# Optimization experiments

Hardware: AMD Instinct MI355X
Metric: run time of the kernel (lower is better)

The kernel has to match this reference:

```python
import jax, jax.numpy as jnp
import numpy as np
from jax import lax

C = 64
K = 3
RED = 8


def _lrelu(x):
    return jax.nn.leaky_relu(x, 0.1)


def setup_inputs() -> dict:
    key = jax.random.key(0)
    ks = jax.random.split(key, 8)
    b, h, w = 32, 128, 128
    x0 = jax.random.normal(ks[0], (b, C, h, w), dtype=jnp.float32)
    v = jax.random.normal(ks[1], (b, C), dtype=jnp.float32)
    s = 0.05
    # CA layer: two 1x1 convs (no bias) acting on the [b,64] embedding
    ca_w1 = jax.random.normal(ks[2], (C // RED, C), dtype=jnp.float32) * s
    ca_w2 = jax.random.normal(ks[3], (C, C // RED), dtype=jnp.float32) * s
    # kernel-generating MLP: Linear(64,64) -> LeakyReLU -> Linear(64, 64*K*K), no bias
    k_w1 = jax.random.normal(ks[4], (C, C), dtype=jnp.float32) * s
    k_w2 = jax.random.normal(ks[5], (C * K * K, C), dtype=jnp.float32) * s
    # final 1x1 conv (default_conv, bias=True)
    conv_w = jax.random.normal(ks[6], (C, C), dtype=jnp.float32) * s
    conv_b = jax.random.normal(ks[7], (C,), dtype=jnp.float32) * s
    return {"x0": x0, "v": v, "ca_w1": ca_w1, "ca_w2": ca_w2,
            "k_w1": k_w1, "k_w2": k_w2, "conv_w": conv_w, "conv_b": conv_b}


def reference(x0, v, ca_w1, ca_w2, k_w1, k_w2, conv_w, conv_b):
    b, c, h, w = x0.shape
    # Channel attention: sigmoid(W2 @ lrelu(W1 @ v)) gates x0 per (b,c)
    att = jax.nn.sigmoid(_lrelu(v @ ca_w1.T) @ ca_w2.T)  # [b, c]
    out = x0 * att[:, :, None, None]
    # Per-sample, per-channel K x K kernels generated from the embedding
    kern = (_lrelu(v @ k_w1.T) @ k_w2.T).reshape(b * c, 1, K, K)
    p = (K - 1) // 2
    y = lax.conv_general_dilated(
        out.reshape(1, b * c, h, w), kern,
        window_strides=(1, 1), padding=[(p, p), (p, p)],
        feature_group_count=b * c,
        dimension_numbers=("NCHW", "OIHW", "NCHW"))
    y = _lrelu(y).reshape(b, c, h, w)
    # final 1x1 conv with bias
    return jnp.einsum("bchw,oc->bohw", y, conv_w) + conv_b[None, :, None, None]
```

## Files before the change

kernel.cpp:

```cpp
#include <hip/hip_runtime.h>

#define HW 128
#define XBb 16
#define XBf 4
#define KTb 24592
#define LDS_BYTES 26896

typedef __attribute__((ext_vector_type(8))) short  bfrag;
typedef __attribute__((ext_vector_type(16))) float f16x;
typedef __attribute__((ext_vector_type(4)))  float f4;

__device__ __forceinline__ float lrelu(float x) { return x > 0.f ? x : 0.1f * x; }

__device__ __forceinline__ short f2bf(float f) {
    unsigned u = __builtin_bit_cast(unsigned, f);
    u = u + 0x7FFFu + ((u >> 16) & 1u);
    return (short)(u >> 16);
}

__device__ float g_ktab[32 * 768];
__device__ short g_whi[4096];

__global__ __launch_bounds__(64) void dgfem_prep(
    const float* __restrict__ v, const float* __restrict__ ca_w1,
    const float* __restrict__ ca_w2, const float* __restrict__ k_w1,
    const float* __restrict__ k_w2, const float* __restrict__ conv_w)
{
    const int b = blockIdx.x;
    const int t = threadIdx.x;

    if (b == 32) {
        for (int i = t; i < 4096; i += 64) g_whi[i] = f2bf(conv_w[i]);
        return;
    }

    __shared__ float vb[64], t1[8], att[64], t2[64];
    vb[t] = v[b * 64 + t];
    __syncthreads();

    if (t < 8) {
        float s = 0.f;
        for (int j = 0; j < 64; ++j) s += vb[j] * ca_w1[t * 64 + j];
        t1[t] = lrelu(s);
    }
    {
        float s = 0.f;
        for (int j = 0; j < 64; ++j) s += vb[j] * k_w1[t * 64 + j];
        t2[t] = lrelu(s);
    }
    __syncthreads();
    {
        float s = 0.f;
        for (int i = 0; i < 8; ++i) s += t1[i] * ca_w2[t * 8 + i];
        att[t] = 1.f / (1.f + expf(-s));
    }
    __syncthreads();
    for (int r = t; r < 576; r += 64) {
        int c = r / 9, tp = r - c * 9;
        float s = 0.f;
        for (int j = 0; j < 64; ++j) s += t2[j] * k_w2[r * 64 + j];
        int m = c >> 4, g = (c >> 3) & 1, a = (c >> 2) & 1, j2 = c & 3;
        int row = ((m * 2 + a) * 2 + g) * 4 + j2;
        int dst = (tp < 4) ? (row * 4 + tp)
                : (tp < 8) ? (256 + row * 4 + (tp - 4))
                           : (512 + row);
        g_ktab[b * 768 + dst] = s * att[c];
    }
}

__global__ __launch_bounds__(256) void dgfem_main(
    const float* __restrict__ x0, const float* __restrict__ conv_b,
    float* __restrict__ out)
{
    const int t  = threadIdx.x;
    const int w  = t >> 6;
    const int l  = t & 63;
    const int g  = l >> 5;
    const int ln = l & 31;
    const int px = w * 32 + ln;

    const int bid  = blockIdx.x;
    const int orig = (bid & 7) * 512 + (bid >> 3);
    const int b    = orig >> 7;
    const int gy   = orig & 127;

    __shared__ __align__(16) char lds[LDS_BYTES];
    float* ldsf = (float*)lds;

    {
        const float* ksrc = g_ktab + b * 768;
        const float rm0 = (gy > 0)   ? 1.f : 0.f;
        const float rm2 = (gy < 127) ? 1.f : 0.f;
        for (int i = t; i < 576; i += 256) {
            float rm;
            if (i < 256)      rm = ((i & 3) < 3) ? rm0 : 1.f;
            else if (i < 512) rm = ((i & 3) < 2) ? 1.f : rm2;
            else              rm = rm2;
            *(float*)(lds + KTb + i * 4) = ksrc[i] * rm;
        }
    }

    const int doff = w * 1024 + l * 16;
    int inv0, inv1, inv2;
    {
        #pragma unroll
        for (int q = 0; q < 3; ++q) {
            int F      = q * 4096 + doff;
            int slot   = F / 1536;
            int within = F - slot * 1536;
            int rowq   = gy - 1 + (within >> 9);
            int crow   = min(max(rowq, 0), 127);
            int gs = slot >> 2, j2s = slot & 3;
            int iv = (gs * 8 + j2s) * 65536 + crow * 512 + (within & 511);
            if (q == 0) inv0 = iv; else if (q == 1) inv1 = iv; else inv2 = iv;
        }
    }

    const char* xb = (const char*)x0 + ((size_t)b << 22);

    #define STAGE(rr_, sel_)                                                   \
    {                                                                          \
        const char* srcb = xb + ((size_t)(((rr_) >> 1) * 16 + ((rr_) & 1) * 4) << 16); \
        char* dstb = lds + XBb + (sel_) * 12288 + doff;                        \
        __builtin_amdgcn_global_load_lds(                                      \
            (const __attribute__((address_space(1))) unsigned*)(srcb + inv0),  \
            (__attribute__((address_space(3))) unsigned*)(dstb), 16, 0, 0);    \
        __builtin_amdgcn_global_load_lds(                                      \
            (const __attribute__((address_space(1))) unsigned*)(srcb + inv1),  \
            (__attribute__((address_space(3))) unsigned*)(dstb + 4096), 16, 0, 0); \
        __builtin_amdgcn_global_load_lds(                                      \
            (const __attribute__((address_space(1))) unsigned*)(srcb + inv2),  \
            (__attribute__((address_space(3))) unsigned*)(dstb + 8192), 16, 0, 0); \
    }

    f16x acc0, acc1;
    #pragma unroll
    for (int i = 0; i < 16; ++i) { acc0[i] = 0.f; acc1[i] = 0.f; }

    const float mLf = (px > 0)   ? 1.f : 0.f;
    const float mRf = (px < 127) ? 1.f : 0.f;

    bfrag yh;
    bfrag whi0, whi1;
    const char* const wbase = (const char*)g_whi + ln * 128 + g * 16;

    STAGE(0, 0);
    __syncthreads();

    #define ROUND(rr_, a_, m_, sel_)                                           \
    {                                                                          \
        if (!(a_)) {                                                           \
            whi0 = *(const bfrag*)(wbase + (m_) * 32);                         \
            whi1 = *(const bfrag*)(wbase + (m_) * 32 + 4096);                  \
        }                                                                      \
        if ((rr_) < 7) STAGE((rr_) + 1, (sel_) ^ 1);                           \
        const float* xbase = ldsf + (XBf + (sel_) * 3072 + g * 1536 + px - 1); \
        const int    krowb = ((rr_) * 2 + g) * 4;                              \
        _Pragma("unroll")                                                      \
        for (int j2 = 0; j2 < 4; ++j2) {                                       \
            f4 kA = *(const f4*)(lds + KTb + (krowb + j2) * 16);               \
            f4 kB = *(const f4*)(lds + KTb + 1024 + (krowb + j2) * 16);        \
            float k8v = *(const float*)(lds + KTb + 2048 + (krowb + j2) * 4);  \
            const float* bA = xbase + j2 * 384;                                \
            float xL0 = bA[0]   * mLf, xC0 = bA[1],   xR0 = bA[2]   * mRf;     \
            float xL1 = bA[128] * mLf, xC1 = bA[129], xR1 = bA[130] * mRf;     \
            float xL2 = bA[256] * mLf, xC2 = bA[257], xR2 = bA[258] * mRf;     \
            float aY = fmaf(kA.x, xL0, fmaf(kA.y, xC0, kA.z * xR0))            \
                     + fmaf(kA.w, xL1, fmaf(kB.x, xC1, kB.y * xR1))            \
                     + fmaf(kB.z, xL2, fmaf(kB.w, xC2, k8v  * xR2));           \
            yh[(a_) * 4 + j2] = f2bf(lrelu(aY));                               \
        }                                                                      \
        if (a_) {                                                              \
            acc0 = __builtin_amdgcn_mfma_f32_32x32x16_bf16(whi0, yh, acc0, 0, 0, 0); \
            acc1 = __builtin_amdgcn_mfma_f32_32x32x16_bf16(whi1, yh, acc1, 0, 0, 0); \
        }                                                                      \
        if ((rr_) < 7) __syncthreads();                                        \
    }

    ROUND(0, 0, 0, 0);
    ROUND(1, 1, 0, 1);
    ROUND(2, 0, 1, 0);
    ROUND(3, 1, 1, 1);
    ROUND(4, 0, 2, 0);
    ROUND(5, 1, 2, 1);
    ROUND(6, 0, 3, 0);
    ROUND(7, 1, 3, 1);

    #undef ROUND
    #undef STAGE

    float* ob = out + ((size_t)b << 20) + (size_t)gy * HW + px;
    #pragma unroll
    for (int q = 0; q < 4; ++q) {
        const int obase = 8 * q + 4 * g;
        float4 bv0 = *(const float4*)&conv_b[obase];
        float4 bv1 = *(const float4*)&conv_b[32 + obase];
        const float* b0f = (const float*)&bv0;
        const float* b1f = (const float*)&bv1;
        #pragma unroll
        for (int r2 = 0; r2 < 4; ++r2) {
            ob[(size_t)(obase + r2) * 16384]      = acc0[q * 4 + r2] + b0f[r2];
            ob[(size_t)(32 + obase + r2) * 16384] = acc1[q * 4 + r2] + b1f[r2];
        }
    }
}

extern "C" void kernel_launch(void* const* d_in, const int* in_sizes, int n_in,
                              void* d_out, int out_size, void* d_ws, size_t ws_size,
                              hipStream_t stream) {
    const float* x0     = (const float*)d_in[0];
    const float* v      = (const float*)d_in[1];
    const float* ca_w1  = (const float*)d_in[2];
    const float* ca_w2  = (const float*)d_in[3];
    const float* k_w1   = (const float*)d_in[4];
    const float* k_w2   = (const float*)d_in[5];
    const float* conv_w = (const float*)d_in[6];
    const float* conv_b = (const float*)d_in[7];
    float* outp = (float*)d_out;

    dgfem_prep<<<dim3(33), dim3(64), 0, stream>>>(v, ca_w1, ca_w2, k_w1, k_w2, conv_w);
    dgfem_main<<<dim3(4096), dim3(256), 0, stream>>>(x0, conv_b, outp);
}
```

Measured before the change: 77.54 us.

## Shrink main kernel to single-wave blocks with barrier-free vmcnt pipelining

Each block now handles one 32-pixel segment of a row with a single 64-lane wave instead of four waves covering the whole row, and the grid grows to match. The x tile per stage becomes a 40-column halo window, and __syncthreads are replaced by explicit s_waitcnt vmcnt on the async global-to-LDS loads. The 1x1 conv weight fragments are also loaded into registers up front. The aim is to drop block-wide barriers and cut LDS use to raise occupancy. In exchange, halo columns are loaded redundantly by neighbouring blocks, the loads are narrower (4-byte ones for the tail), and there are more blocks to schedule.

```diff
diff --git a/kernel.cpp b/kernel.cpp
--- a/kernel.cpp
+++ b/kernel.cpp
@@ -1,10 +1,8 @@
 #include <hip/hip_runtime.h>
 
 #define HW 128
-#define XBb 16
-#define XBf 4
-#define KTb 24592
-#define LDS_BYTES 26896
+#define XBB 2304
+#define LDS_BYTES 10016
 
 typedef __attribute__((ext_vector_type(8))) short  bfrag;
 typedef __attribute__((ext_vector_type(16))) float f16x;
@@ -68,21 +66,21 @@
     }
 }
 
-__global__ __launch_bounds__(256) void dgfem_main(
+__global__ __launch_bounds__(64) void dgfem_main(
     const float* __restrict__ x0, const float* __restrict__ conv_b,
     float* __restrict__ out)
 {
-    const int t  = threadIdx.x;
-    const int w  = t >> 6;
-    const int l  = t & 63;
+    const int l  = threadIdx.x;
     const int g  = l >> 5;
     const int ln = l & 31;
-    const int px = w * 32 + ln;
 
     const int bid  = blockIdx.x;
-    const int orig = (bid & 7) * 512 + (bid >> 3);
-    const int b    = orig >> 7;
-    const int gy   = orig & 127;
+    const int orig = (bid & 7) * 2048 + (bid >> 3);
+    const int b    = orig >> 9;
+    const int rem  = orig & 511;
+    const int gy   = rem >> 2;
+    const int px0  = (rem & 3) * 32;
+    const int px   = px0 + ln;
 
     __shared__ __align__(16) char lds[LDS_BYTES];
     float* ldsf = (float*)lds;
@@ -91,28 +89,30 @@
         const float* ksrc = g_ktab + b * 768;
         const float rm0 = (gy > 0)   ? 1.f : 0.f;
         const float rm2 = (gy < 127) ? 1.f : 0.f;
-        for (int i = t; i < 576; i += 256) {
+        for (int i = l; i < 576; i += 64) {
             float rm;
             if (i < 256)      rm = ((i & 3) < 3) ? rm0 : 1.f;
             else if (i < 512) rm = ((i & 3) < 2) ? 1.f : rm2;
             else              rm = rm2;
-            *(float*)(lds + KTb + i * 4) = ksrc[i] * rm;
-        }
-    }
-
-    const int doff = w * 1024 + l * 16;
-    int inv0, inv1, inv2;
+            ldsf[i] = ksrc[i] * rm;
+        }
+    }
+
+    const int ws  = min(max(px0 * 4 - 16, 0), 352);
+    const int ADJ = px0 - (ws >> 2) - 1;
+
+    int s0, s1, s2, s3, s4, s5;
     {
         #pragma unroll
-        for (int q = 0; q < 3; ++q) {
-            int F      = q * 4096 + doff;
-            int slot   = F / 1536;
-            int within = F - slot * 1536;
-            int rowq   = gy - 1 + (within >> 9);
-            int crow   = min(max(rowq, 0), 127);
-            int gs = slot >> 2, j2s = slot & 3;
-            int iv = (gs * 8 + j2s) * 65536 + crow * 512 + (within & 511);
-            if (q == 0) inv0 = iv; else if (q == 1) inv1 = iv; else inv2 = iv;
+        for (int q = 0; q < 6; ++q) {
+            int F     = (q < 3) ? (q * 1024 + l * 16) : (3072 + (q - 3) * 256 + l * 4);
+            int ch    = F / 480, wq = F - ch * 480;
+            int chsrc = (ch >> 2) * 8 + (ch & 3);
+            int row   = wq / 160, colb = wq - row * 160;
+            int crow  = min(max(gy - 1 + row, 0), 127);
+            int iv    = chsrc * 65536 + crow * 512 + ws + colb;
+            if (q == 0) s0 = iv; else if (q == 1) s1 = iv; else if (q == 2) s2 = iv;
+            else if (q == 3) s3 = iv; else if (q == 4) s4 = iv; else s5 = iv;
         }
     }
 
@@ -121,16 +121,25 @@
     #define STAGE(rr_, sel_)                                                   \
     {                                                                          \
         const char* srcb = xb + ((size_t)(((rr_) >> 1) * 16 + ((rr_) & 1) * 4) << 16); \
-        char* dstb = lds + XBb + (sel_) * 12288 + doff;                        \
-        __builtin_amdgcn_global_load_lds(                                      \
-            (const __attribute__((address_space(1))) unsigned*)(srcb + inv0),  \
+        char* dstb = lds + XBB + (sel_) * 3840;                                \
+        __builtin_amdgcn_global_load_lds(                                      \
+            (const __attribute__((address_space(1))) unsigned*)(srcb + s0),    \
             (__attribute__((address_space(3))) unsigned*)(dstb), 16, 0, 0);    \
         __builtin_amdgcn_global_load_lds(                                      \
-            (const __attribute__((address_space(1))) unsigned*)(srcb + inv1),  \
-            (__attribute__((address_space(3))) unsigned*)(dstb + 4096), 16, 0, 0); \
-        __builtin_amdgcn_global_load_lds(                                      \
-            (const __attribute__((address_space(1))) unsigned*)(srcb + inv2),  \
-            (__attribute__((address_space(3))) unsigned*)(dstb + 8192), 16, 0, 0); \
+            (const __attribute__((address_space(1))) unsigned*)(srcb + s1),    \
+            (__attribute__((address_space(3))) unsigned*)(dstb + 1024), 16, 0, 0); \
+        __builtin_amdgcn_global_load_lds(                                      \
+            (const __attribute__((address_space(1))) unsigned*)(srcb + s2),    \
+            (__attribute__((address_space(3))) unsigned*)(dstb + 2048), 16, 0, 0); \
+        __builtin_amdgcn_global_load_lds(                                      \
+            (const __attribute__((address_space(1))) unsigned*)(srcb + s3),    \
+            (__attribute__((address_space(3))) unsigned*)(dstb + 3072), 4, 0, 0); \
+        __builtin_amdgcn_global_load_lds(                                      \
+            (const __attribute__((address_space(1))) unsigned*)(srcb + s4),    \
+            (__attribute__((address_space(3))) unsigned*)(dstb + 3328), 4, 0, 0); \
+        __builtin_amdgcn_global_load_lds(                                      \
+            (const __attribute__((address_space(1))) unsigned*)(srcb + s5),    \
+            (__attribute__((address_space(3))) unsigned*)(dstb + 3584), 4, 0, 0); \
     }
 
     f16x acc0, acc1;
@@ -141,40 +150,48 @@
     const float mRf = (px < 127) ? 1.f : 0.f;
 
     bfrag yh;
-    bfrag whi0, whi1;
-    const char* const wbase = (const char*)g_whi + ln * 128 + g * 16;
-
+
+    bfrag wh0[4], wh1[4];
+    {
+        const char* wbase = (const char*)g_whi + ln * 128 + g * 16;
+        #pragma unroll
+        for (int m = 0; m < 4; ++m) {
+            wh0[m] = *(const bfrag*)(wbase + m * 32);
+            wh1[m] = *(const bfrag*)(wbase + m * 32 + 4096);
+        }
+    }
+    __builtin_amdgcn_sched_barrier(0);
     STAGE(0, 0);
-    __syncthreads();
 
     #define ROUND(rr_, a_, m_, sel_)                                           \
     {                                                                          \
-        if (!(a_)) {                                                           \
-            whi0 = *(const bfrag*)(wbase + (m_) * 32);                         \
-            whi1 = *(const bfrag*)(wbase + (m_) * 32 + 4096);                  \
+        if ((rr_) < 7) {                                                       \
+            STAGE((rr_) + 1, (sel_) ^ 1);                                      \
+            asm volatile("s_waitcnt vmcnt(6)" ::: "memory");                   \
+        } else {                                                               \
+            asm volatile("s_waitcnt vmcnt(0)" ::: "memory");                   \
         }                                                                      \
-        if ((rr_) < 7) STAGE((rr_) + 1, (sel_) ^ 1);                           \
-        const float* xbase = ldsf + (XBf + (sel_) * 3072 + g * 1536 + px - 1); \
+        __builtin_amdgcn_sched_barrier(0);                                     \
+        const float* xbase = ldsf + (576 + (sel_) * 960 + g * 480 + ln + ADJ); \
         const int    krowb = ((rr_) * 2 + g) * 4;                              \
         _Pragma("unroll")                                                      \
         for (int j2 = 0; j2 < 4; ++j2) {                                       \
-            f4 kA = *(const f4*)(lds + KTb + (krowb + j2) * 16);               \
-            f4 kB = *(const f4*)(lds + KTb + 1024 + (krowb + j2) * 16);        \
-            float k8v = *(const float*)(lds + KTb + 2048 + (krowb + j2) * 4);  \
-            const float* bA = xbase + j2 * 384;                                \
-            float xL0 = bA[0]   * mLf, xC0 = bA[1],   xR0 = bA[2]   * mRf;     \
-            float xL1 = bA[128] * mLf, xC1 = bA[129], xR1 = bA[130] * mRf;     \
-            float xL2 = bA[256] * mLf, xC2 = bA[257], xR2 = bA[258] * mRf;     \
+            f4 kA = *(const f4*)(lds + (krowb + j2) * 16);                     \
+            f4 kB = *(const f4*)(lds + 1024 + (krowb + j2) * 16);              \
+            float k8v = *(const float*)(lds + 2048 + (krowb + j2) * 4);        \
+            const float* bA = xbase + j2 * 120;                                \
+            float xL0 = bA[0]  * mLf, xC0 = bA[1],  xR0 = bA[2]  * mRf;        \
+            float xL1 = bA[40] * mLf, xC1 = bA[41], xR1 = bA[42] * mRf;        \
+            float xL2 = bA[80] * mLf, xC2 = bA[81], xR2 = bA[82] * mRf;        \
             float aY = fmaf(kA.x, xL0, fmaf(kA.y, xC0, kA.z * xR0))            \
                      + fmaf(kA.w, xL1, fmaf(kB.x, xC1, kB.y * xR1))            \
                      + fmaf(kB.z, xL2, fmaf(kB.w, xC2, k8v  * xR2));           \
             yh[(a_) * 4 + j2] = f2bf(lrelu(aY));                               \
         }                                                                      \
         if (a_) {                                                              \
-            acc0 = __builtin_amdgcn_mfma_f32_32x32x16_bf16(whi0, yh, acc0, 0, 0, 0); \
-            acc1 = __builtin_amdgcn_mfma_f32_32x32x16_bf16(whi1, yh, acc1, 0, 0, 0); \
+            acc0 = __builtin_amdgcn_mfma_f32_32x32x16_bf16(wh0[m_], yh, acc0, 0, 0, 0); \
+            acc1 = __builtin_amdgcn_mfma_f32_32x32x16_bf16(wh1[m_], yh, acc1, 0, 0, 0); \
         }                                                                      \
-        if ((rr_) < 7) __syncthreads();                                        \
     }
 
     ROUND(0, 0, 0, 0);
@@ -219,5 +236,5 @@
     float* outp = (float*)d_out;
 
     dgfem_prep<<<dim3(33), dim3(64), 0, stream>>>(v, ca_w1, ca_w2, k_w1, k_w2, conv_w);
-    dgfem_main<<<dim3(4096), dim3(256), 0, stream>>>(x0, conv_b, outp);
-}
+    dgfem_main<<<dim3(16384), dim3(64), 0, stream>>>(x0, conv_b, outp);
+}
```

After: 96.37 us. +24.3%, slower.

## Deepen LDS staging from double to triple buffering with explicit vmcnt waits

Applied to the files above, without the earlier changes.

The x-tile staging ring grows from two LDS buffers to three, and each round now prefetches two rounds ahead instead of one. Full __syncthreads are replaced by explicit s_waitcnt vmcnt counts plus s_barrier, with sched_barrier fences around them. This gives global-to-LDS loads more time in flight before they are consumed. In exchange LDS use per block rises, which may lower occupancy, and the hand-counted vmcnt values must exactly match the number of outstanding loads.

```diff
diff --git a/kernel.cpp b/kernel.cpp
--- a/kernel.cpp
+++ b/kernel.cpp
@@ -3,8 +3,8 @@
 #define HW 128
 #define XBb 16
 #define XBf 4
-#define KTb 24592
-#define LDS_BYTES 26896
+#define KTb 36880
+#define LDS_BYTES 39184
 
 typedef __attribute__((ext_vector_type(8))) short  bfrag;
 typedef __attribute__((ext_vector_type(16))) float f16x;
@@ -118,10 +118,10 @@
 
     const char* xb = (const char*)x0 + ((size_t)b << 22);
 
-    #define STAGE(rr_, sel_)                                                   \
+    #define STAGE(rr_, s3_)                                                    \
     {                                                                          \
         const char* srcb = xb + ((size_t)(((rr_) >> 1) * 16 + ((rr_) & 1) * 4) << 16); \
-        char* dstb = lds + XBb + (sel_) * 12288 + doff;                        \
+        char* dstb = lds + XBb + (s3_) * 12288 + doff;                         \
         __builtin_amdgcn_global_load_lds(                                      \
             (const __attribute__((address_space(1))) unsigned*)(srcb + inv0),  \
             (__attribute__((address_space(3))) unsigned*)(dstb), 16, 0, 0);    \
@@ -145,15 +145,19 @@
     const char* const wbase = (const char*)g_whi + ln * 128 + g * 16;
 
     STAGE(0, 0);
-    __syncthreads();
-
-    #define ROUND(rr_, a_, m_, sel_)                                           \
+    STAGE(1, 1);
+    __builtin_amdgcn_sched_barrier(0);
+    asm volatile("s_waitcnt vmcnt(3) lgkmcnt(0)" ::: "memory");
+    __builtin_amdgcn_s_barrier();
+    __builtin_amdgcn_sched_barrier(0);
+
+    #define ROUND(rr_, a_, m_, sel_, stg_, B_)                                 \
     {                                                                          \
         if (!(a_)) {                                                           \
             whi0 = *(const bfrag*)(wbase + (m_) * 32);                         \
             whi1 = *(const bfrag*)(wbase + (m_) * 32 + 4096);                  \
         }                                                                      \
-        if ((rr_) < 7) STAGE((rr_) + 1, (sel_) ^ 1);                           \
+        if ((rr_) < 6) STAGE((rr_) + 2, stg_);                                 \
         const float* xbase = ldsf + (XBf + (sel_) * 3072 + g * 1536 + px - 1); \
         const int    krowb = ((rr_) * 2 + g) * 4;                              \
         _Pragma("unroll")                                                      \
@@ -174,17 +178,22 @@
             acc0 = __builtin_amdgcn_mfma_f32_32x32x16_bf16(whi0, yh, acc0, 0, 0, 0); \
             acc1 = __builtin_amdgcn_mfma_f32_32x32x16_bf16(whi1, yh, acc1, 0, 0, 0); \
         }                                                                      \
-        if ((rr_) < 7) __syncthreads();                                        \
-    }
-
-    ROUND(0, 0, 0, 0);
-    ROUND(1, 1, 0, 1);
-    ROUND(2, 0, 1, 0);
-    ROUND(3, 1, 1, 1);
-    ROUND(4, 0, 2, 0);
-    ROUND(5, 1, 2, 1);
-    ROUND(6, 0, 3, 0);
-    ROUND(7, 1, 3, 1);
+        if ((rr_) < 7) {                                                       \
+            __builtin_amdgcn_sched_barrier(0);                                 \
+            asm volatile("s_waitcnt vmcnt(" #B_ ")" ::: "memory");             \
+            __builtin_amdgcn_s_barrier();                                      \
+            __builtin_amdgcn_sched_barrier(0);                                 \
+        }                                                                      \
+    }
+
+    ROUND(0, 0, 0, 0, 2, 5);
+    ROUND(1, 1, 0, 1, 0, 3);
+    ROUND(2, 0, 1, 2, 1, 5);
+    ROUND(3, 1, 1, 0, 2, 3);
+    ROUND(4, 0, 2, 1, 0, 5);
+    ROUND(5, 1, 2, 2, 1, 3);
+    ROUND(6, 0, 3, 0, 0, 2);
+    ROUND(7, 1, 3, 1, 0, 0);
 
     #undef ROUND
     #undef STAGE
```

Result: slower. 85.44 us (+10.2%).
